# Optimization experiments

Measured on AMD Instinct MI355X. Metric: run time of the kernel, lower is better.

The kernel has to match this reference:

```python
import jax, jax.numpy as jnp
import numpy as np

EPS = 1e-5

def bn_relu(y, g, b):
    # BatchNorm1d in training mode: stats over (B, L) per channel, biased variance
    mu = jnp.mean(y, axis=(0, 2), keepdims=True)
    var = jnp.var(y, axis=(0, 2), keepdims=True)
    yn = (y - mu) * jax.lax.rsqrt(var + EPS)
    return jax.nn.relu(yn * g[None, :, None] + b[None, :, None])

def conv1x1_pad1(x, W):
    # Conv1d(k=1, padding=1, bias=False): pointwise matmul then zero-pad length by 1 each side
    y = jnp.einsum('bcl,oc->bol', x, W)
    return jnp.pad(y, ((0, 0), (0, 0), (1, 1)))

def conv1x1(x, W, b):
    return jnp.einsum('bcl,oc->bol', x, W) + b[None, :, None]

def conv3_pad1(x, W):
    # Conv1d(k=3, padding=1, bias=False); W: [O, C, 3]
    return jax.lax.conv_general_dilated(x, W, window_strides=(1,), padding=((1, 1),),
                                        dimension_numbers=('NCH', 'OIH', 'NCH'))

def pam(f, Wq, bq, Wk, bk, Wv, bv, gamma):
    q = conv1x1(f, Wq, bq)          # [B, C//8, L]
    k = conv1x1(f, Wk, bk)          # [B, C//8, L]
    v = conv1x1(f, Wv, bv)          # [B, C, L]
    energy = jnp.einsum('bql,bqm->blm', q, k)   # [B, L, L]
    attn = jax.nn.softmax(energy, axis=-1)
    out = jnp.einsum('bcm,blm->bcl', v, attn)
    return gamma * out + f

def cam(f, gamma):
    energy = jnp.einsum('bcl,bdl->bcd', f, f)    # [B, C, C]
    energy_new = jnp.max(energy, axis=-1, keepdims=True) - energy
    attn = jax.nn.softmax(energy_new, axis=-1)
    out = jnp.einsum('bcd,bdl->bcl', attn, f)
    return gamma * out + f

def setup_inputs() -> dict:
    key = jax.random.key(0)
    ks = jax.random.split(key, 24)
    B, C, L = 8, 256, 2046
    IC, OC = C // 4, 128  # inter_channels=64, out_channels
    s = 0.05
    d = {
        'x':   jax.random.normal(ks[0], (B, C, L), jnp.float32),
        'W5a': jax.random.normal(ks[1], (IC, C), jnp.float32) * s,
        'g5a': jnp.ones((IC,), jnp.float32), 'b5a': jnp.zeros((IC,), jnp.float32),
        'W5c': jax.random.normal(ks[2], (IC, C), jnp.float32) * s,
        'g5c': jnp.ones((IC,), jnp.float32), 'b5c': jnp.zeros((IC,), jnp.float32),
        'Wq':  jax.random.normal(ks[3], (IC // 8, IC), jnp.float32) * s,
        'bq':  jnp.zeros((IC // 8,), jnp.float32),
        'Wk':  jax.random.normal(ks[4], (IC // 8, IC), jnp.float32) * s,
        'bk':  jnp.zeros((IC // 8,), jnp.float32),
        'Wv':  jax.random.normal(ks[5], (IC, IC), jnp.float32) * s,
        'bv':  jnp.zeros((IC,), jnp.float32),
        'gamma_pam': jnp.full((1,), 0.1, jnp.float32),
        'gamma_cam': jnp.full((1,), 0.1, jnp.float32),
        'W51': jax.random.normal(ks[6], (IC, IC, 3), jnp.float32) * s,
        'g51': jnp.ones((IC,), jnp.float32), 'b51': jnp.zeros((IC,), jnp.float32),
        'W52': jax.random.normal(ks[7], (IC, IC, 3), jnp.float32) * s,
        'g52': jnp.ones((IC,), jnp.float32), 'b52': jnp.zeros((IC,), jnp.float32),
        'W6':  jax.random.normal(ks[8], (OC, IC), jnp.float32) * s,
        'b6':  jnp.zeros((OC,), jnp.float32),
        'W7':  jax.random.normal(ks[9], (OC, IC), jnp.float32) * s,
        'b7':  jnp.zeros((OC,), jnp.float32),
        'W8':  jax.random.normal(ks[10], (OC, IC), jnp.float32) * s,
        'b8':  jnp.zeros((OC,), jnp.float32),
    }
    return d

def reference(x, W5a, g5a, b5a, W5c, g5c, b5c, Wq, bq, Wk, bk, Wv, bv,
              gamma_pam, gamma_cam, W51, g51, b51, W52, g52, b52,
              W6, b6, W7, b7, W8, b8):
    # dropout (p=0.1) treated as identity (eval mode)
    feat1 = bn_relu(conv1x1_pad1(x, W5a), g5a, b5a)          # [B, IC, L+2]
    sa_feat = pam(feat1, Wq, bq, Wk, bk, Wv, bv, gamma_pam)
    sa_conv = bn_relu(conv3_pad1(sa_feat, W51), g51, b51)
    sa_output = conv1x1(sa_conv, W6, b6)                     # [B, OC, L+2]
    feat2 = bn_relu(conv1x1_pad1(x, W5c), g5c, b5c)
    sc_feat = cam(feat2, gamma_cam)
    sc_conv = bn_relu(conv3_pad1(sc_feat, W52), g52, b52)
    sc_output = conv1x1(sc_conv, W7, b7)
    feat_sum = sa_conv + sc_conv
    sasc = conv1x1(feat_sum, W8, b8)
    # pool == 'maxpool' selects AdaptiveAvgPool1d(1) in the original (note swap)
    sasc = jnp.mean(sasc, axis=-1)                            # [B, OC]
    return (sasc, sa_output, sc_output)
```

## Files before the change

kernel.cpp:

```cpp
#include <hip/hip_runtime.h>
#include <math.h>

#define B 8
#define C 256
#define L 2046
#define LP 2048
#define IC 64
#define OC 128
#define BN_EPS 1e-5f
#define INVN (1.f / 16384.f)

#define OFF_Y1T    0u
#define OFF_Y2C    524288u
#define OFF_SAFT   1048576u
#define OFF_SCFT   1572864u
#define OFF_Y51T   2097152u
#define OFF_Y52T   2621440u
#define OFF_VB     3145728u
#define OFF_QT     3670016u
#define OFF_KT     3735552u
#define OFF_LPART  3801088u
#define OFF_EPART  3866624u
#define OFF_ATTN   4390912u
#define OFF_PART1  4423680u
#define OFF_PART2  4489216u
#define OFF_COEF1  4554752u
#define OFF_COEF2  4555008u
#define OFF_FSUM   4555264u
#define OFF_W5BF   4555776u
#define OFF_W67    4572160u
#define OFF_WT     4580352u
#define OFF_WQKV   4592640u
#define OFF_BQKV   4595200u

typedef __attribute__((ext_vector_type(8))) short bshort8;
typedef __attribute__((ext_vector_type(4))) float f32x4;

__device__ __forceinline__ unsigned short f2bf(float f) {
    union { float f; unsigned int u; } v; v.f = f;
    unsigned int r = v.u + 0x7fffu + ((v.u >> 16) & 1u);
    return (unsigned short)(r >> 16);
}
__device__ __forceinline__ float bf2f(unsigned short u) {
    union { unsigned int i; float f; } v; v.i = ((unsigned int)u) << 16;
    return v.f;
}
__device__ __forceinline__ unsigned int pk2(float a, float b) {
    return (unsigned int)f2bf(a) | ((unsigned int)f2bf(b) << 16);
}

__global__ __launch_bounds__(256) void k_wprep(
        const float* __restrict__ W5a, const float* __restrict__ W5c,
        const float* __restrict__ W6, const float* __restrict__ W7,
        const float* __restrict__ W51, const float* __restrict__ W52,
        const float* __restrict__ Wq, const float* __restrict__ Wk,
        const float* __restrict__ Wv, const float* __restrict__ bq,
        const float* __restrict__ bk, const float* __restrict__ bv,
        unsigned short* __restrict__ W5BF, unsigned short* __restrict__ W67,
        unsigned short* __restrict__ WT, unsigned short* __restrict__ WQKV,
        float* __restrict__ BQKV, float* __restrict__ FSUM) {
    int i = blockIdx.x * 256 + threadIdx.x;
    if (i < 32768) {
        int o = i >> 8, c = i & 255;
        W5BF[i] = f2bf(o < 64 ? W5a[o * 256 + c] : W5c[(o - 64) * 256 + c]);
    } else if (i < 49152) {
        int j = i - 32768; int g = j >> 13; int r = j & 8191;
        W67[j] = f2bf(g ? W7[r] : W6[r]);
    } else if (i < 73728) {
        int j = i - 49152;
        int c = j & 63, o = (j >> 6) & 63, wt = j >> 12; int w = wt / 3, t = wt % 3;
        const float* Ws = w ? W52 : W51;
        WT[j] = f2bf(Ws[(o * 64 + c) * 3 + t]);
    } else if (i < 78848) {
        int j = i - 73728; int o = j >> 6, c = j & 63;
        float v = o < 8 ? Wq[o * 64 + c] : (o < 16 ? Wk[(o - 8) * 64 + c] : Wv[(o - 16) * 64 + c]);
        WQKV[j] = f2bf(v);
    } else if (i < 78928) {
        int o = i - 78848;
        BQKV[o] = o < 8 ? bq[o] : (o < 16 ? bk[o - 8] : bv[o - 16]);
    } else if (i < 79440) {
        FSUM[i - 78928] = 0.f;
    }
}

__global__ __launch_bounds__(256) void k_conv1(const float* __restrict__ x,
        const unsigned short* __restrict__ W5BF,
        unsigned short* __restrict__ Y1T, unsigned short* __restrict__ Y2C,
        float* __restrict__ PART1) {
    __shared__ float lds_part[4][128];
    int lt = blockIdx.x, og = blockIdx.y, b = blockIdx.z;
    int w = threadIdx.x >> 6, lane = threadIdx.x & 63;
    int n = lane & 15, quad = lane >> 4;
    int lp = lt * 64 + w * 16 + n;
    int ls = lp - 1;
    bool valid = (ls >= 0) && (ls < L);
    f32x4 acc[4];
#pragma unroll
    for (int ot = 0; ot < 4; ++ot) acc[ot] = (f32x4){0.f, 0.f, 0.f, 0.f};
    for (int ck = 0; ck < 8; ++ck) {
        int c0 = ck * 32 + quad * 8;
        bshort8 xb = {};
        if (valid) {
            const float* xs = x + ((size_t)(b * C + c0)) * L + ls;
#pragma unroll
            for (int j = 0; j < 8; ++j)
                ((unsigned short*)&xb)[j] = f2bf(xs[(size_t)j * L]);
        }
#pragma unroll
        for (int ot = 0; ot < 4; ++ot) {
            bshort8 wf = *(const bshort8*)(W5BF + (size_t)(og * 64 + ot * 16 + n) * C + ck * 32 + quad * 8);
            acc[ot] = __builtin_amdgcn_mfma_f32_16x16x32_bf16(wf, xb, acc[ot], 0, 0, 0);
        }
    }
    if (og == 0) {
#pragma unroll
        for (int ot = 0; ot < 4; ++ot) {
            uint2 pv;
            pv.x = pk2(acc[ot][0], acc[ot][1]);
            pv.y = pk2(acc[ot][2], acc[ot][3]);
            *(uint2*)(Y1T + ((size_t)(b * LP + lp)) * IC + ot * 16 + quad * 4) = pv;
        }
    } else {
#pragma unroll
        for (int ot = 0; ot < 4; ++ot)
#pragma unroll
            for (int r = 0; r < 4; ++r) {
                int o = ot * 16 + quad * 4 + r;
                Y2C[((size_t)(b * IC + o)) * LP + lp] = f2bf(acc[ot][r]);
            }
    }
#pragma unroll
    for (int ot = 0; ot < 4; ++ot)
#pragma unroll
        for (int r = 0; r < 4; ++r) {
            float s = acc[ot][r], q = s * s;
#pragma unroll
            for (int msk = 1; msk < 16; msk <<= 1) {
                s += __shfl_xor(s, msk, 64);
                q += __shfl_xor(q, msk, 64);
            }
            if (n == 0) {
                int ch = ot * 16 + quad * 4 + r;
                lds_part[w][ch * 2] = s;
                lds_part[w][ch * 2 + 1] = q;
            }
        }
    __syncthreads();
    int t = threadIdx.x;
    if (t < 128) {
        float s = lds_part[0][t] + lds_part[1][t] + lds_part[2][t] + lds_part[3][t];
        PART1[(size_t)(og * 128 + t) * 256 + (b * 32 + lt)] = s;
    }
}

__global__ __launch_bounds__(256) void k_red(const float* __restrict__ PART,
        const float* __restrict__ g0, const float* __restrict__ b0,
        const float* __restrict__ g1, const float* __restrict__ b1,
        float* __restrict__ COEF) {
    int ch = blockIdx.x;
    int t = threadIdx.x;
    float s = PART[(size_t)(ch * 2) * 256 + t];
    float q = PART[(size_t)(ch * 2 + 1) * 256 + t];
    for (int off = 32; off; off >>= 1) {
        s += __shfl_down(s, off, 64);
        q += __shfl_down(q, off, 64);
    }
    __shared__ float rs[4], rq[4];
    if ((t & 63) == 0) { rs[t >> 6] = s; rq[t >> 6] = q; }
    __syncthreads();
    if (t == 0) {
        float S = rs[0] + rs[1] + rs[2] + rs[3];
        float Q = rq[0] + rq[1] + rq[2] + rq[3];
        float mu = S * INVN;
        float var = Q * INVN - mu * mu;
        float gv = ch < 64 ? g0[ch] : g1[ch - 64];
        float bv = ch < 64 ? b0[ch] : b1[ch - 64];
        float A = gv * rsqrtf(var + BN_EPS);
        COEF[ch * 2] = A;
        COEF[ch * 2 + 1] = bv - mu * A;
    }
}

__global__ __launch_bounds__(256) void k_qkv(const unsigned short* __restrict__ Y1T,
        const float* __restrict__ COEF1,
        const unsigned short* __restrict__ WQKV, const float* __restrict__ BQKV,
        unsigned short* __restrict__ QT, unsigned short* __restrict__ KT,
        unsigned short* __restrict__ VB) {
    __shared__ float cA[64], cB[64];
    int lt = blockIdx.x, b = blockIdx.y;
    int t = threadIdx.x;
    if (t < 64) { cA[t] = COEF1[t * 2]; cB[t] = COEF1[t * 2 + 1]; }
    __syncthreads();
    int w = t >> 6, lane = t & 63, n = lane & 15, quad = lane >> 4;
    int lrow = lt * 64 + w * 16 + n;
    bshort8 fb[2];
#pragma unroll
    for (int kt = 0; kt < 2; ++kt) {
        bshort8 raw = *(const bshort8*)(Y1T + ((size_t)(b * LP + lrow)) * IC + kt * 32 + quad * 8);
        bshort8 f;
#pragma unroll
        for (int j = 0; j < 8; ++j) {
            int c = kt * 32 + quad * 8 + j;
            float v = fmaf(cA[c], bf2f((unsigned short)raw[j]), cB[c]);
            v = fmaxf(v, 0.f);
            ((unsigned short*)&f)[j] = f2bf(v);
        }
        fb[kt] = f;
    }
    f32x4 acc[5];
#pragma unroll
    for (int ot = 0; ot < 5; ++ot) {
        f32x4 a = {0.f, 0.f, 0.f, 0.f};
#pragma unroll
        for (int kt = 0; kt < 2; ++kt) {
            bshort8 wf = *(const bshort8*)(WQKV + (size_t)(ot * 16 + n) * IC + kt * 32 + quad * 8);
            a = __builtin_amdgcn_mfma_f32_16x16x32_bf16(wf, fb[kt], a, 0, 0, 0);
        }
        acc[ot] = a;
    }
#pragma unroll
    for (int ot = 0; ot < 5; ++ot)
#pragma unroll
        for (int r = 0; r < 4; ++r) {
            int o = ot * 16 + quad * 4 + r;
            unsigned short bv16 = f2bf(acc[ot][r] + BQKV[o]);
            if (ot == 0) {
                if (o < 8) QT[((size_t)(b * LP + lrow)) * 8 + o] = bv16;
                else KT[((size_t)(b * LP + lrow)) * 8 + (o - 8)] = bv16;
            } else {
                VB[((size_t)(b * IC + (o - 16))) * LP + lrow] = bv16;
            }
        }
}

__global__ __launch_bounds__(256) void k_pam(
        const unsigned short* __restrict__ qT, const unsigned short* __restrict__ kT,
        const unsigned short* __restrict__ vb,
        unsigned short* __restrict__ OPART, float* __restrict__ LPART) {
    __shared__ unsigned char smem[18432];
    unsigned short* vs = (unsigned short*)smem;
    unsigned short* ps = vs + 4608;
    float* os = (float*)smem;
    int qt = blockIdx.x, ks = blockIdx.y, b = blockIdx.z;
    int l0 = qt * 64;
    int tid = threadIdx.x;
    int wq = tid >> 6, lane = tid & 63, n = lane & 15, quad = lane >> 4;
    bshort8 qa = {};
    if (quad == 0)
        qa = *(const bshort8*)(qT + ((size_t)(b * LP + l0 + wq * 16 + n)) * 8);
    f32x4 acc[4];
#pragma unroll
    for (int s = 0; s < 4; ++s) acc[s] = (f32x4){0.f, 0.f, 0.f, 0.f};
    float li[4] = {0.f, 0.f, 0.f, 0.f};
    unsigned short* pw = ps + wq * 16 * 72;

    for (int it = 0; it < 8; ++it) {
        int m0 = ks * 512 + it * 64;
        __syncthreads();
        {
            int row = tid >> 2, chn = tid & 3;
            const unsigned short* src = vb + ((size_t)(b * IC + row)) * LP + m0 + chn * 16;
            unsigned short* dstl = vs + row * 72 + chn * 16;
            *(bshort8*)dstl = *(const bshort8*)src;
            *(bshort8*)(dstl + 8) = *(const bshort8*)(src + 8);
        }
        bshort8 kb[4];
#pragma unroll
        for (int s = 0; s < 4; ++s) kb[s] = (bshort8){};
        if (quad == 0) {
#pragma unroll
            for (int s = 0; s < 4; ++s)
                kb[s] = *(const bshort8*)(kT + ((size_t)(b * LP + m0 + s * 16 + n)) * 8);
        }
        __syncthreads();
        f32x4 sc[4];
#pragma unroll
        for (int s = 0; s < 4; ++s)
            sc[s] = __builtin_amdgcn_mfma_f32_16x16x32_bf16(qa, kb[s],
                        (f32x4){0.f, 0.f, 0.f, 0.f}, 0, 0, 0);
#pragma unroll
        for (int s = 0; s < 4; ++s)
#pragma unroll
            for (int r = 0; r < 4; ++r) {
                float p = __expf(sc[s][r]);
                li[r] += p;
                pw[(quad * 4 + r) * 72 + s * 16 + n] = f2bf(p);
            }
#pragma unroll
        for (int step = 0; step < 2; ++step) {
            bshort8 pa = *(const bshort8*)(pw + n * 72 + step * 32 + quad * 8);
#pragma unroll
            for (int s = 0; s < 4; ++s) {
                bshort8 vf = *(const bshort8*)(vs + (s * 16 + n) * 72 + step * 32 + quad * 8);
                acc[s] = __builtin_amdgcn_mfma_f32_16x16x32_bf16(pa, vf, acc[s], 0, 0, 0);
            }
        }
    }
    __syncthreads();
#pragma unroll
    for (int s = 0; s < 4; ++s)
#pragma unroll
        for (int r = 0; r < 4; ++r)
            os[(s * 16 + n) * 65 + wq * 16 + quad * 4 + r] = acc[s][r];
    size_t lbase = ((size_t)((b * 32 + qt) * 4 + ks)) * 64;
#pragma unroll
    for (int r = 0; r < 4; ++r) {
        float s_ = li[r];
#pragma unroll
        for (int msk = 1; msk < 16; msk <<= 1) s_ += __shfl_xor(s_, msk, 64);
        if (n == 0) LPART[lbase + wq * 16 + quad * 4 + r] = s_;
    }
    __syncthreads();
    size_t ob = ((size_t)((b * 32 + qt) * 4 + ks)) * 4096;
    int c = tid >> 2, qc = tid & 3;
    unsigned int* od = (unsigned int*)(OPART + ob + c * 64 + qc * 16);
#pragma unroll
    for (int i = 0; i < 8; ++i)
        od[i] = pk2(os[c * 65 + qc * 16 + 2 * i], os[c * 65 + qc * 16 + 2 * i + 1]);
}

__global__ __launch_bounds__(256) void k_pam_combine(
        const unsigned short* __restrict__ OPART, const float* __restrict__ LPART,
        const unsigned short* __restrict__ Y1T, const float* __restrict__ COEF1,
        const float* __restrict__ gamma, unsigned short* __restrict__ SAFT) {
    __shared__ float dn[64];
    __shared__ float cA[64], cB[64];
    __shared__ unsigned short tile[64 * 66];
    int qt = blockIdx.x, b = blockIdx.y;
    int l0 = qt * 64;
    int t = threadIdx.x;
    if (t < 64) {
        cA[t] = COEF1[t * 2]; cB[t] = COEF1[t * 2 + 1];
        size_t lbase = ((size_t)((b * 32 + qt) * 4)) * 64;
        dn[t] = LPART[lbase + t] + LPART[lbase + 64 + t] +
                LPART[lbase + 128 + t] + LPART[lbase + 192 + t];
    }
    __syncthreads();
    int c = t >> 2, qc = t & 3;
    float O[16];
#pragma unroll
    for (int i = 0; i < 16; ++i) O[i] = 0.f;
    size_t ob = ((size_t)((b * 32 + qt) * 4)) * 4096 + c * 64 + qc * 16;
#pragma unroll
    for (int s = 0; s < 4; ++s) {
        bshort8 p0 = *(const bshort8*)(OPART + ob + (size_t)s * 4096);
        bshort8 p1 = *(const bshort8*)(OPART + ob + (size_t)s * 4096 + 8);
#pragma unroll
        for (int i = 0; i < 8; ++i) {
            O[i]     += bf2f((unsigned short)p0[i]);
            O[8 + i] += bf2f((unsigned short)p1[i]);
        }
    }
    float gm = gamma[0];
#pragma unroll
    for (int i = 0; i < 16; ++i) {
        int q = qc * 16 + i;
        unsigned short raw = Y1T[((size_t)(b * LP + l0 + q)) * IC + c];
        float f1v = fmaxf(fmaf(cA[c], bf2f(raw), cB[c]), 0.f);
        float val = fmaf(gm, O[i] / dn[q], f1v);
        tile[q * 66 + c] = f2bf(val);
    }
    __syncthreads();
    int li = t >> 2, cc = t & 3;
    unsigned int* dst = (unsigned int*)(SAFT + ((size_t)(b * LP + l0 + li)) * IC + cc * 16);
#pragma unroll
    for (int i = 0; i < 8; ++i)
        dst[i] = *(unsigned int*)(tile + li * 66 + cc * 16 + 2 * i);
}

__global__ __launch_bounds__(256) void k_gram(const unsigned short* __restrict__ Y2C,
        const float* __restrict__ COEF1, float* __restrict__ EPART) {
    __shared__ float fs[64][132];
    __shared__ float cA[64], cB[64];
    int b = blockIdx.y;
    int l0 = blockIdx.x * 128;
    int t = threadIdx.x;
    if (t < 64) { cA[t] = COEF1[(64 + t) * 2]; cB[t] = COEF1[(64 + t) * 2 + 1]; }
    __syncthreads();
    for (int i = t; i < 64 * 64; i += 256) {
        int c = i >> 6, i2 = i & 63;
        unsigned int u = *(const unsigned int*)(Y2C + ((size_t)(b * IC + c)) * LP + l0 + i2 * 2);
        float A = cA[c], Bc = cB[c];
        fs[c][i2 * 2]     = fmaxf(fmaf(A, bf2f((unsigned short)u), Bc), 0.f);
        fs[c][i2 * 2 + 1] = fmaxf(fmaf(A, bf2f((unsigned short)(u >> 16)), Bc), 0.f);
    }
    __syncthreads();
    int c = t >> 2, dg = t & 3;
    float acc[16];
#pragma unroll
    for (int i = 0; i < 16; ++i) acc[i] = 0.f;
    for (int i4 = 0; i4 < 32; ++i4) {
        const float4 fc = *reinterpret_cast<const float4*>(&fs[c][i4 * 4]);
#pragma unroll
        for (int dd = 0; dd < 16; ++dd) {
            const float4 fd = *reinterpret_cast<const float4*>(&fs[dg * 16 + dd][i4 * 4]);
            acc[dd] += fc.x * fd.x + fc.y * fd.y + fc.z * fd.z + fc.w * fd.w;
        }
    }
    size_t base = ((size_t)(b * 16 + blockIdx.x)) * 4096 + c * 64 + dg * 16;
    for (int dd = 0; dd < 16; ++dd)
        EPART[base + dd] = acc[dd];
}

__global__ __launch_bounds__(256) void k_cam_softmax(const float* __restrict__ EPART,
        float* __restrict__ attn) {
    __shared__ float e[4096];
    int b = blockIdx.x, t = threadIdx.x;
    for (int idx = t; idx < 4096; idx += 256) {
        float s = 0.f;
        for (int ch = 0; ch < 16; ++ch) s += EPART[((size_t)(b * 16 + ch)) * 4096 + idx];
        e[idx] = s;
    }
    __syncthreads();
    if (t < 64) {
        float mn = INFINITY;
        for (int d = 0; d < 64; ++d) mn = fminf(mn, e[t * 64 + d]);
        float s = 0.f;
        float* a = attn + (size_t)b * 4096 + t * 64;
        for (int d = 0; d < 64; ++d) { float p = __expf(mn - e[t * 64 + d]); a[d] = p; s += p; }
        float inv = 1.f / s;
        for (int d = 0; d < 64; ++d) a[d] *= inv;
    }
}

__global__ __launch_bounds__(256) void k_cam_apply(const float* __restrict__ attn,
        const unsigned short* __restrict__ Y2C, const float* __restrict__ COEF1,
        const float* __restrict__ gamma, unsigned short* __restrict__ SCFT) {
    __shared__ __align__(16) float as[64 * 64];
    __shared__ float cA[64], cB[64];
    __shared__ unsigned short tile[128 * 66];
    int b = blockIdx.y;
    int l0 = blockIdx.x * 128;
    int t = threadIdx.x;
    int lq = t & 127, ch = t >> 7;
    if (t < 64) { cA[t] = COEF1[(64 + t) * 2]; cB[t] = COEF1[(64 + t) * 2 + 1]; }
    for (int i = t; i < 4096; i += 256) as[i] = attn[(size_t)b * 4096 + i];
    __syncthreads();
    float acc[32];
#pragma unroll
    for (int i = 0; i < 32; ++i) acc[i] = 0.f;
    const unsigned short* fb = Y2C + (size_t)b * IC * LP + l0 + lq;
    for (int d4 = 0; d4 < 16; ++d4) {
        float fv[4];
#pragma unroll
        for (int i = 0; i < 4; ++i) {
            int d = 4 * d4 + i;
            fv[i] = fmaxf(fmaf(cA[d], bf2f(fb[(size_t)d * LP]), cB[d]), 0.f);
        }
#pragma unroll
        for (int cc = 0; cc < 32; ++cc) {
            const float4 a4 = *reinterpret_cast<const float4*>(as + (ch * 32 + cc) * 64 + d4 * 4);
            acc[cc] += a4.x * fv[0] + a4.y * fv[1] + a4.z * fv[2] + a4.w * fv[3];
        }
    }
    float gm = gamma[0];
#pragma unroll
    for (int cc = 0; cc < 32; ++cc) {
        int c = ch * 32 + cc;
        float res = fmaxf(fmaf(cA[c], bf2f(fb[(size_t)c * LP]), cB[c]), 0.f);
        tile[lq * 66 + c] = f2bf(fmaf(gm, acc[cc], res));
    }
    __syncthreads();
    int li = t >> 1, half = t & 1;
    unsigned int* dst = (unsigned int*)(SCFT + ((size_t)(b * LP + l0 + li)) * IC + half * 32);
#pragma unroll
    for (int i = 0; i < 16; ++i)
        dst[i] = *(unsigned int*)(tile + li * 66 + half * 32 + 2 * i);
}

__global__ __launch_bounds__(256) void k_conv3(const unsigned short* __restrict__ SAFT,
        const unsigned short* __restrict__ SCFT, const unsigned short* __restrict__ WTall,
        unsigned short* __restrict__ Y51T, unsigned short* __restrict__ Y52T,
        float* __restrict__ PART2) {
    __shared__ float lds_part[4][128];
    int lt = blockIdx.x, og = blockIdx.y, b = blockIdx.z;
    const unsigned short* FTsrc = og ? SCFT : SAFT;
    const unsigned short* WT = WTall + og * 12288;
    unsigned short* dst = og ? Y52T : Y51T;
    int l0 = lt * 64;
    int w = threadIdx.x >> 6, lane = threadIdx.x & 63, n = lane & 15, quad = lane >> 4;
    int lrow = l0 + w * 16 + n;
    f32x4 acc[4];
#pragma unroll
    for (int ot = 0; ot < 4; ++ot) acc[ot] = (f32x4){0.f, 0.f, 0.f, 0.f};
#pragma unroll
    for (int t3 = 0; t3 < 3; ++t3) {
        int row = lrow + t3 - 1;
        bshort8 fb[2];
#pragma unroll
        for (int kt = 0; kt < 2; ++kt) {
            if (row >= 0 && row < LP)
                fb[kt] = *(const bshort8*)(FTsrc + ((size_t)(b * LP + row)) * IC + kt * 32 + quad * 8);
            else fb[kt] = (bshort8){};
        }
#pragma unroll
        for (int ot = 0; ot < 4; ++ot)
#pragma unroll
            for (int kt = 0; kt < 2; ++kt) {
                bshort8 wf = *(const bshort8*)(WT + ((size_t)(t3 * 64 + ot * 16 + n)) * IC + kt * 32 + quad * 8);
                acc[ot] = __builtin_amdgcn_mfma_f32_16x16x32_bf16(wf, fb[kt], acc[ot], 0, 0, 0);
            }
    }
#pragma unroll
    for (int ot = 0; ot < 4; ++ot) {
        uint2 pv;
        pv.x = pk2(acc[ot][0], acc[ot][1]);
        pv.y = pk2(acc[ot][2], acc[ot][3]);
        *(uint2*)(dst + ((size_t)(b * LP + lrow)) * IC + ot * 16 + quad * 4) = pv;
    }
#pragma unroll
    for (int ot = 0; ot < 4; ++ot)
#pragma unroll
        for (int r = 0; r < 4; ++r) {
            float s = acc[ot][r], q = s * s;
#pragma unroll
            for (int msk = 1; msk < 16; msk <<= 1) {
                s += __shfl_xor(s, msk, 64);
                q += __shfl_xor(q, msk, 64);
            }
            if (n == 0) {
                int cch = ot * 16 + quad * 4 + r;
                lds_part[w][cch * 2] = s;
                lds_part[w][cch * 2 + 1] = q;
            }
        }
    __syncthreads();
    int t = threadIdx.x;
    if (t < 128) {
        float s = lds_part[0][t] + lds_part[1][t] + lds_part[2][t] + lds_part[3][t];
        PART2[(size_t)(og * 128 + t) * 256 + (b * 32 + lt)] = s;
    }
}

__global__ __launch_bounds__(256) void k_final(const unsigned short* __restrict__ Y51T,
        const unsigned short* __restrict__ Y52T, const float* __restrict__ COEF2,
        const unsigned short* __restrict__ W67,
        const float* __restrict__ b6, const float* __restrict__ b7,
        float* __restrict__ out_sa, float* __restrict__ out_sc,
        float* __restrict__ FSUM) {
    __shared__ float cA[128], cB[128];
    __shared__ float fsw[4][64];
    int lt = blockIdx.x, og = blockIdx.y, b = blockIdx.z;
    int t = threadIdx.x;
    if (t < 128) { cA[t] = COEF2[t * 2]; cB[t] = COEF2[t * 2 + 1]; }
    __syncthreads();
    int w = t >> 6, lane = t & 63, n = lane & 15, quad = lane >> 4;
    int lrow = lt * 64 + w * 16 + n;
    float fs_lane[16];
    bshort8 ba[2], bb[2];
#pragma unroll
    for (int kt = 0; kt < 2; ++kt) {
        bshort8 ra = *(const bshort8*)(Y51T + ((size_t)(b * LP + lrow)) * IC + kt * 32 + quad * 8);
        bshort8 rb = *(const bshort8*)(Y52T + ((size_t)(b * LP + lrow)) * IC + kt * 32 + quad * 8);
        bshort8 fa, fb;
#pragma unroll
        for (int j = 0; j < 8; ++j) {
            int c = kt * 32 + quad * 8 + j;
            float v1 = fmaxf(fmaf(cA[c], bf2f((unsigned short)ra[j]), cB[c]), 0.f);
            float v2 = fmaxf(fmaf(cA[64 + c], bf2f((unsigned short)rb[j]), cB[64 + c]), 0.f);
            ((unsigned short*)&fa)[j] = f2bf(v1);
            ((unsigned short*)&fb)[j] = f2bf(v2);
            fs_lane[kt * 8 + j] = v1 + v2;
        }
        ba[kt] = fa; bb[kt] = fb;
    }
    f32x4 accA[4], accB[4];
#pragma unroll
    for (int ot = 0; ot < 4; ++ot) {
        accA[ot] = (f32x4){0.f, 0.f, 0.f, 0.f};
        accB[ot] = (f32x4){0.f, 0.f, 0.f, 0.f};
    }
#pragma unroll
    for (int ot = 0; ot < 4; ++ot)
#pragma unroll
        for (int kt = 0; kt < 2; ++kt) {
            bshort8 wa = *(const bshort8*)(W67 + (size_t)(og * 64 + ot * 16 + n) * IC + kt * 32 + quad * 8);
            bshort8 wb = *(const bshort8*)(W67 + 8192 + (size_t)(og * 64 + ot * 16 + n) * IC + kt * 32 + quad * 8);
            accA[ot] = __builtin_amdgcn_mfma_f32_16x16x32_bf16(wa, ba[kt], accA[ot], 0, 0, 0);
            accB[ot] = __builtin_amdgcn_mfma_f32_16x16x32_bf16(wb, bb[kt], accB[ot], 0, 0, 0);
        }
#pragma unroll
    for (int ot = 0; ot < 4; ++ot)
#pragma unroll
        for (int r = 0; r < 4; ++r) {
            int o = og * 64 + ot * 16 + quad * 4 + r;
            out_sa[((size_t)(b * OC + o)) * LP + lrow] = accA[ot][r] + b6[o];
            out_sc[((size_t)(b * OC + o)) * LP + lrow] = accB[ot][r] + b7[o];
        }
    if (og == 0) {
#pragma unroll
        for (int i = 0; i < 16; ++i) {
            float s = fs_lane[i];
#pragma unroll
            for (int msk = 1; msk < 16; msk <<= 1) s += __shfl_xor(s, msk, 64);
            if (n == 0) {
                int c = (i >> 3) * 32 + quad * 8 + (i & 7);
                fsw[w][c] = s;
            }
        }
        __syncthreads();
        if (t < 64)
            atomicAdd(&FSUM[b * 64 + t], fsw[0][t] + fsw[1][t] + fsw[2][t] + fsw[3][t]);
    }
}

__global__ __launch_bounds__(128) void k_sasc(const float* __restrict__ FSUM,
        const float* __restrict__ W8, const float* __restrict__ b8,
        float* __restrict__ out) {
    __shared__ float mean[64];
    int b = blockIdx.x, t = threadIdx.x;
    if (t < 64) mean[t] = FSUM[b * 64 + t] * (1.f / (float)LP);
    __syncthreads();
    float s = b8[t];
    for (int c = 0; c < 64; ++c) s = fmaf(W8[t * 64 + c], mean[c], s);
    out[b * OC + t] = s;
}

extern "C" void kernel_launch(void* const* d_in, const int* in_sizes, int n_in,
                              void* d_out, int out_size, void* d_ws, size_t ws_size,
                              hipStream_t stream) {
    (void)in_sizes; (void)n_in; (void)out_size; (void)ws_size;
    const float* x    = (const float*)d_in[0];
    const float* W5a  = (const float*)d_in[1];
    const float* g5a  = (const float*)d_in[2];
    const float* b5a  = (const float*)d_in[3];
    const float* W5c  = (const float*)d_in[4];
    const float* g5c  = (const float*)d_in[5];
    const float* b5c  = (const float*)d_in[6];
    const float* Wq   = (const float*)d_in[7];
    const float* bq   = (const float*)d_in[8];
    const float* Wk   = (const float*)d_in[9];
    const float* bk   = (const float*)d_in[10];
    const float* Wv   = (const float*)d_in[11];
    const float* bv   = (const float*)d_in[12];
    const float* gpam = (const float*)d_in[13];
    const float* gcam = (const float*)d_in[14];
    const float* W51  = (const float*)d_in[15];
    const float* g51  = (const float*)d_in[16];
    const float* b51  = (const float*)d_in[17];
    const float* W52  = (const float*)d_in[18];
    const float* g52  = (const float*)d_in[19];
    const float* b52  = (const float*)d_in[20];
    const float* W6   = (const float*)d_in[21];
    const float* b6   = (const float*)d_in[22];
    const float* W7   = (const float*)d_in[23];
    const float* b7   = (const float*)d_in[24];
    const float* W8   = (const float*)d_in[25];
    const float* b8   = (const float*)d_in[26];

    float* ws = (float*)d_ws;
    float* out = (float*)d_out;
    unsigned short* Y1T  = (unsigned short*)(ws + OFF_Y1T);
    unsigned short* Y2C  = (unsigned short*)(ws + OFF_Y2C);
    unsigned short* SAFT = (unsigned short*)(ws + OFF_SAFT);
    unsigned short* SCFT = (unsigned short*)(ws + OFF_SCFT);
    unsigned short* Y51T = (unsigned short*)(ws + OFF_Y51T);
    unsigned short* Y52T = (unsigned short*)(ws + OFF_Y52T);
    unsigned short* VB   = (unsigned short*)(ws + OFF_VB);
    unsigned short* QT   = (unsigned short*)(ws + OFF_QT);
    unsigned short* KT   = (unsigned short*)(ws + OFF_KT);
    float* LPART  = ws + OFF_LPART;
    float* EPART  = ws + OFF_EPART;
    float* ATTN   = ws + OFF_ATTN;
    float* PART1  = ws + OFF_PART1;
    float* PART2  = ws + OFF_PART2;
    float* COEF1  = ws + OFF_COEF1;
    float* COEF2  = ws + OFF_COEF2;
    float* FSUM   = ws + OFF_FSUM;
    unsigned short* W5BF = (unsigned short*)(ws + OFF_W5BF);
    unsigned short* W67  = (unsigned short*)(ws + OFF_W67);
    unsigned short* WT   = (unsigned short*)(ws + OFF_WT);
    unsigned short* WQKV = (unsigned short*)(ws + OFF_WQKV);
    float* BQKV = ws + OFF_BQKV;

    float* out_sa = out + B * OC;
    float* out_sc = out + B * OC + (size_t)B * OC * LP;
    unsigned short* OPART = (unsigned short*)out_sa;

    k_wprep<<<311, 256, 0, stream>>>(W5a, W5c, W6, W7, W51, W52, Wq, Wk, Wv,
                                     bq, bk, bv, W5BF, W67, WT, WQKV, BQKV, FSUM);
    k_conv1<<<dim3(32, 2, B), 256, 0, stream>>>(x, W5BF, Y1T, Y2C, PART1);
    k_red<<<128, 256, 0, stream>>>(PART1, g5a, b5a, g5c, b5c, COEF1);
    k_qkv<<<dim3(32, B), 256, 0, stream>>>(Y1T, COEF1, WQKV, BQKV, QT, KT, VB);
    k_pam<<<dim3(32, 4, B), 256, 0, stream>>>(QT, KT, VB, OPART, LPART);
    k_pam_combine<<<dim3(32, B), 256, 0, stream>>>(OPART, LPART, Y1T, COEF1, gpam, SAFT);
    k_gram<<<dim3(16, B), 256, 0, stream>>>(Y2C, COEF1, EPART);
    k_cam_softmax<<<B, 256, 0, stream>>>(EPART, ATTN);
    k_cam_apply<<<dim3(16, B), 256, 0, stream>>>(ATTN, Y2C, COEF1, gcam, SCFT);
    k_conv3<<<dim3(32, 2, B), 256, 0, stream>>>(SAFT, SCFT, WT, Y51T, Y52T, PART2);
    k_red<<<128, 256, 0, stream>>>(PART2, g51, b51, g52, b52, COEF2);
    k_final<<<dim3(32, 2, B), 256, 0, stream>>>(Y51T, Y52T, COEF2, W67, b6, b7,
                                                out_sa, out_sc, FSUM);
    k_sasc<<<B, 128, 0, stream>>>(FSUM, W8, b8, out);
}
```

Baseline: 243.4 us.

## Fuse independent PAM/CAM stages into shared launches and drop reduction kernels

Replaces the per-tile BN partial buffers and the two k_red kernels with atomic accumulation of channel sums, with each consumer computing the BN coefficients itself. Independent PAM and CAM work (qkv+gram, pam+cam_softmax, pam_combine+cam_apply) now runs as role-dispatched blocks inside single launches using dynamic shared memory. The gram step is rewritten to use bf16 MFMA instead of fp32 FMA, and the final sasc mean is folded into k_final via atomics. Together these cut the launch count from 13 to 7 and let independent branches fill the GPU concurrently. In exchange, float atomics make the sums order-nondeterministic and the bf16 gram adds rounding error.

Result: faster. 233.5 us (-4.1%).

```diff
diff --git a/kernel.cpp b/kernel.cpp
--- a/kernel.cpp
+++ b/kernel.cpp
@@ -22,16 +22,13 @@
 #define OFF_LPART  3801088u
 #define OFF_EPART  3866624u
 #define OFF_ATTN   4390912u
-#define OFF_PART1  4423680u
-#define OFF_PART2  4489216u
-#define OFF_COEF1  4554752u
-#define OFF_COEF2  4555008u
-#define OFF_FSUM   4555264u
-#define OFF_W5BF   4555776u
-#define OFF_W67    4572160u
-#define OFF_WT     4580352u
-#define OFF_WQKV   4592640u
-#define OFF_BQKV   4595200u
+#define OFF_STATS1 4423680u
+#define OFF_STATS2 4423936u
+#define OFF_W5BF   4424192u
+#define OFF_W67    4440576u
+#define OFF_WT     4448768u
+#define OFF_WQKV   4461056u
+#define OFF_BQKV   4463616u
 
 typedef __attribute__((ext_vector_type(8))) short bshort8;
 typedef __attribute__((ext_vector_type(4))) float f32x4;
@@ -47,6 +44,20 @@
 }
 __device__ __forceinline__ unsigned int pk2(float a, float b) {
     return (unsigned int)f2bf(a) | ((unsigned int)f2bf(b) << 16);
+}
+
+__device__ __forceinline__ void load_coef(const float* __restrict__ STATS,
+        const float* __restrict__ g, const float* __restrict__ beta,
+        int base, int cnt, float* cA, float* cB) {
+    int t = threadIdx.x;
+    if (t < cnt) {
+        float s = STATS[(base + t) * 2], q = STATS[(base + t) * 2 + 1];
+        float mu = s * INVN;
+        float var = q * INVN - mu * mu;
+        float A = g[t] * rsqrtf(var + BN_EPS);
+        cA[t] = A;
+        cB[t] = beta[t] - mu * A;
+    }
 }
 
 __global__ __launch_bounds__(256) void k_wprep(
@@ -56,9 +67,11 @@
         const float* __restrict__ Wq, const float* __restrict__ Wk,
         const float* __restrict__ Wv, const float* __restrict__ bq,
         const float* __restrict__ bk, const float* __restrict__ bv,
+        const float* __restrict__ b8,
         unsigned short* __restrict__ W5BF, unsigned short* __restrict__ W67,
         unsigned short* __restrict__ WT, unsigned short* __restrict__ WQKV,
-        float* __restrict__ BQKV, float* __restrict__ FSUM) {
+        float* __restrict__ BQKV, float* __restrict__ STATS1,
+        float* __restrict__ STATS2, float* __restrict__ out_sasc) {
     int i = blockIdx.x * 256 + threadIdx.x;
     if (i < 32768) {
         int o = i >> 8, c = i & 255;
@@ -76,17 +89,21 @@
         float v = o < 8 ? Wq[o * 64 + c] : (o < 16 ? Wk[(o - 8) * 64 + c] : Wv[(o - 16) * 64 + c]);
         WQKV[j] = f2bf(v);
     } else if (i < 78928) {
-        int o = i - 78848;
+        int o = i - 73728 - 5120;
         BQKV[o] = o < 8 ? bq[o] : (o < 16 ? bk[o - 8] : bv[o - 16]);
     } else if (i < 79440) {
-        FSUM[i - 78928] = 0.f;
+        int j = i - 78928;
+        if (j < 256) STATS1[j] = 0.f; else STATS2[j - 256] = 0.f;
+    } else if (i < 80464) {
+        int j = i - 79440;
+        out_sasc[j] = b8[j & 127];
     }
 }
 
 __global__ __launch_bounds__(256) void k_conv1(const float* __restrict__ x,
         const unsigned short* __restrict__ W5BF,
         unsigned short* __restrict__ Y1T, unsigned short* __restrict__ Y2C,
-        float* __restrict__ PART1) {
+        float* __restrict__ STATS1) {
     __shared__ float lds_part[4][128];
     int lt = blockIdx.x, og = blockIdx.y, b = blockIdx.z;
     int w = threadIdx.x >> 6, lane = threadIdx.x & 63;
@@ -149,48 +166,21 @@
     int t = threadIdx.x;
     if (t < 128) {
         float s = lds_part[0][t] + lds_part[1][t] + lds_part[2][t] + lds_part[3][t];
-        PART1[(size_t)(og * 128 + t) * 256 + (b * 32 + lt)] = s;
-    }
-}
-
-__global__ __launch_bounds__(256) void k_red(const float* __restrict__ PART,
-        const float* __restrict__ g0, const float* __restrict__ b0,
-        const float* __restrict__ g1, const float* __restrict__ b1,
-        float* __restrict__ COEF) {
-    int ch = blockIdx.x;
-    int t = threadIdx.x;
-    float s = PART[(size_t)(ch * 2) * 256 + t];
-    float q = PART[(size_t)(ch * 2 + 1) * 256 + t];
-    for (int off = 32; off; off >>= 1) {
-        s += __shfl_down(s, off, 64);
-        q += __shfl_down(q, off, 64);
-    }
-    __shared__ float rs[4], rq[4];
-    if ((t & 63) == 0) { rs[t >> 6] = s; rq[t >> 6] = q; }
-    __syncthreads();
-    if (t == 0) {
-        float S = rs[0] + rs[1] + rs[2] + rs[3];
-        float Q = rq[0] + rq[1] + rq[2] + rq[3];
-        float mu = S * INVN;
-        float var = Q * INVN - mu * mu;
-        float gv = ch < 64 ? g0[ch] : g1[ch - 64];
-        float bv = ch < 64 ? b0[ch] : b1[ch - 64];
-        float A = gv * rsqrtf(var + BN_EPS);
-        COEF[ch * 2] = A;
-        COEF[ch * 2 + 1] = bv - mu * A;
-    }
-}
-
-__global__ __launch_bounds__(256) void k_qkv(const unsigned short* __restrict__ Y1T,
-        const float* __restrict__ COEF1,
+        atomicAdd(&STATS1[og * 128 + t], s);
+    }
+}
+
+__device__ void role_qkv(char* dynsm, int lt, int b,
+        const unsigned short* __restrict__ Y1T, const float* __restrict__ STATS1,
+        const float* __restrict__ g5a, const float* __restrict__ b5a,
         const unsigned short* __restrict__ WQKV, const float* __restrict__ BQKV,
         unsigned short* __restrict__ QT, unsigned short* __restrict__ KT,
         unsigned short* __restrict__ VB) {
-    __shared__ float cA[64], cB[64];
-    int lt = blockIdx.x, b = blockIdx.y;
-    int t = threadIdx.x;
-    if (t < 64) { cA[t] = COEF1[t * 2]; cB[t] = COEF1[t * 2 + 1]; }
-    __syncthreads();
+    float* cA = (float*)dynsm;
+    float* cB = cA + 64;
+    load_coef(STATS1, g5a, b5a, 0, 64, cA, cB);
+    __syncthreads();
+    int t = threadIdx.x;
     int w = t >> 6, lane = t & 63, n = lane & 15, quad = lane >> 4;
     int lrow = lt * 64 + w * 16 + n;
     bshort8 fb[2];
@@ -201,8 +191,7 @@
 #pragma unroll
         for (int j = 0; j < 8; ++j) {
             int c = kt * 32 + quad * 8 + j;
-            float v = fmaf(cA[c], bf2f((unsigned short)raw[j]), cB[c]);
-            v = fmaxf(v, 0.f);
+            float v = fmaxf(fmaf(cA[c], bf2f((unsigned short)raw[j]), cB[c]), 0.f);
             ((unsigned short*)&f)[j] = f2bf(v);
         }
         fb[kt] = f;
@@ -233,15 +222,73 @@
         }
 }
 
-__global__ __launch_bounds__(256) void k_pam(
+__device__ void role_gram(char* dynsm, int blk, int b,
+        const unsigned short* __restrict__ Y2C, const float* __restrict__ STATS1,
+        const float* __restrict__ g5c, const float* __restrict__ b5c,
+        float* __restrict__ EPART) {
+    float* cA = (float*)dynsm;
+    float* cB = cA + 64;
+    load_coef(STATS1, g5c, b5c, 64, 64, cA, cB);
+    __syncthreads();
+    int t = threadIdx.x;
+    int w = t >> 6, lane = t & 63, n = lane & 15, quad = lane >> 4;
+    f32x4 acc[4][4];
+#pragma unroll
+    for (int ti = 0; ti < 4; ++ti)
+#pragma unroll
+        for (int tj = 0; tj < 4; ++tj) acc[ti][tj] = (f32x4){0.f, 0.f, 0.f, 0.f};
+    for (int chunk = 0; chunk < 4; ++chunk) {
+        int lb = (blk * 4 + w) * 128 + chunk * 32 + quad * 8;
+        bshort8 frag[4];
+#pragma unroll
+        for (int g = 0; g < 4; ++g) {
+            int c = g * 16 + n;
+            bshort8 raw = *(const bshort8*)(Y2C + ((size_t)(b * IC + c)) * LP + lb);
+            bshort8 f;
+            float A = cA[c], Bc = cB[c];
+#pragma unroll
+            for (int j = 0; j < 8; ++j)
+                ((unsigned short*)&f)[j] = f2bf(fmaxf(fmaf(A, bf2f((unsigned short)raw[j]), Bc), 0.f));
+            frag[g] = f;
+        }
+#pragma unroll
+        for (int ti = 0; ti < 4; ++ti)
+#pragma unroll
+            for (int tj = 0; tj < 4; ++tj)
+                acc[ti][tj] = __builtin_amdgcn_mfma_f32_16x16x32_bf16(frag[ti], frag[tj], acc[ti][tj], 0, 0, 0);
+    }
+    float* ep = EPART + ((size_t)(b * 16 + blk * 4 + w)) * 4096;
+#pragma unroll
+    for (int ti = 0; ti < 4; ++ti)
+#pragma unroll
+        for (int tj = 0; tj < 4; ++tj)
+#pragma unroll
+            for (int r = 0; r < 4; ++r)
+                ep[(ti * 16 + quad * 4 + r) * 64 + tj * 16 + n] = acc[ti][tj][r];
+}
+
+__global__ __launch_bounds__(256) void k_fuse1(
+        const unsigned short* __restrict__ Y1T, const unsigned short* __restrict__ Y2C,
+        const float* __restrict__ STATS1,
+        const float* __restrict__ g5a, const float* __restrict__ b5a,
+        const float* __restrict__ g5c, const float* __restrict__ b5c,
+        const unsigned short* __restrict__ WQKV, const float* __restrict__ BQKV,
+        unsigned short* __restrict__ QT, unsigned short* __restrict__ KT,
+        unsigned short* __restrict__ VB, float* __restrict__ EPART) {
+    extern __shared__ char dynsm[];
+    int idx = blockIdx.x;
+    if (idx < 256) role_qkv(dynsm, idx & 31, idx >> 5, Y1T, STATS1, g5a, b5a,
+                            WQKV, BQKV, QT, KT, VB);
+    else { int g = idx - 256; role_gram(dynsm, g & 3, g >> 2, Y2C, STATS1, g5c, b5c, EPART); }
+}
+
+__device__ void role_pam(char* dynsm, int qt, int ks, int b,
         const unsigned short* __restrict__ qT, const unsigned short* __restrict__ kT,
         const unsigned short* __restrict__ vb,
         unsigned short* __restrict__ OPART, float* __restrict__ LPART) {
-    __shared__ unsigned char smem[18432];
-    unsigned short* vs = (unsigned short*)smem;
+    unsigned short* vs = (unsigned short*)dynsm;
     unsigned short* ps = vs + 4608;
-    float* os = (float*)smem;
-    int qt = blockIdx.x, ks = blockIdx.y, b = blockIdx.z;
+    float* os = (float*)dynsm;
     int l0 = qt * 64;
     int tid = threadIdx.x;
     int wq = tid >> 6, lane = tid & 63, n = lane & 15, quad = lane >> 4;
@@ -319,93 +366,10 @@
         od[i] = pk2(os[c * 65 + qc * 16 + 2 * i], os[c * 65 + qc * 16 + 2 * i + 1]);
 }
 
-__global__ __launch_bounds__(256) void k_pam_combine(
-        const unsigned short* __restrict__ OPART, const float* __restrict__ LPART,
-        const unsigned short* __restrict__ Y1T, const float* __restrict__ COEF1,
-        const float* __restrict__ gamma, unsigned short* __restrict__ SAFT) {
-    __shared__ float dn[64];
-    __shared__ float cA[64], cB[64];
-    __shared__ unsigned short tile[64 * 66];
-    int qt = blockIdx.x, b = blockIdx.y;
-    int l0 = qt * 64;
-    int t = threadIdx.x;
-    if (t < 64) {
-        cA[t] = COEF1[t * 2]; cB[t] = COEF1[t * 2 + 1];
-        size_t lbase = ((size_t)((b * 32 + qt) * 4)) * 64;
-        dn[t] = LPART[lbase + t] + LPART[lbase + 64 + t] +
-                LPART[lbase + 128 + t] + LPART[lbase + 192 + t];
-    }
-    __syncthreads();
-    int c = t >> 2, qc = t & 3;
-    float O[16];
-#pragma unroll
-    for (int i = 0; i < 16; ++i) O[i] = 0.f;
-    size_t ob = ((size_t)((b * 32 + qt) * 4)) * 4096 + c * 64 + qc * 16;
-#pragma unroll
-    for (int s = 0; s < 4; ++s) {
-        bshort8 p0 = *(const bshort8*)(OPART + ob + (size_t)s * 4096);
-        bshort8 p1 = *(const bshort8*)(OPART + ob + (size_t)s * 4096 + 8);
-#pragma unroll
-        for (int i = 0; i < 8; ++i) {
-            O[i]     += bf2f((unsigned short)p0[i]);
-            O[8 + i] += bf2f((unsigned short)p1[i]);
-        }
-    }
-    float gm = gamma[0];
-#pragma unroll
-    for (int i = 0; i < 16; ++i) {
-        int q = qc * 16 + i;
-        unsigned short raw = Y1T[((size_t)(b * LP + l0 + q)) * IC + c];
-        float f1v = fmaxf(fmaf(cA[c], bf2f(raw), cB[c]), 0.f);
-        float val = fmaf(gm, O[i] / dn[q], f1v);
-        tile[q * 66 + c] = f2bf(val);
-    }
-    __syncthreads();
-    int li = t >> 2, cc = t & 3;
-    unsigned int* dst = (unsigned int*)(SAFT + ((size_t)(b * LP + l0 + li)) * IC + cc * 16);
-#pragma unroll
-    for (int i = 0; i < 8; ++i)
-        dst[i] = *(unsigned int*)(tile + li * 66 + cc * 16 + 2 * i);
-}
-
-__global__ __launch_bounds__(256) void k_gram(const unsigned short* __restrict__ Y2C,
-        const float* __restrict__ COEF1, float* __restrict__ EPART) {
-    __shared__ float fs[64][132];
-    __shared__ float cA[64], cB[64];
-    int b = blockIdx.y;
-    int l0 = blockIdx.x * 128;
-    int t = threadIdx.x;
-    if (t < 64) { cA[t] = COEF1[(64 + t) * 2]; cB[t] = COEF1[(64 + t) * 2 + 1]; }
-    __syncthreads();
-    for (int i = t; i < 64 * 64; i += 256) {
-        int c = i >> 6, i2 = i & 63;
-        unsigned int u = *(const unsigned int*)(Y2C + ((size_t)(b * IC + c)) * LP + l0 + i2 * 2);
-        float A = cA[c], Bc = cB[c];
-        fs[c][i2 * 2]     = fmaxf(fmaf(A, bf2f((unsigned short)u), Bc), 0.f);
-        fs[c][i2 * 2 + 1] = fmaxf(fmaf(A, bf2f((unsigned short)(u >> 16)), Bc), 0.f);
-    }
-    __syncthreads();
-    int c = t >> 2, dg = t & 3;
-    float acc[16];
-#pragma unroll
-    for (int i = 0; i < 16; ++i) acc[i] = 0.f;
-    for (int i4 = 0; i4 < 32; ++i4) {
-        const float4 fc = *reinterpret_cast<const float4*>(&fs[c][i4 * 4]);
-#pragma unroll
-        for (int dd = 0; dd < 16; ++dd) {
-            const float4 fd = *reinterpret_cast<const float4*>(&fs[dg * 16 + dd][i4 * 4]);
-            acc[dd] += fc.x * fd.x + fc.y * fd.y + fc.z * fd.z + fc.w * fd.w;
-        }
-    }
-    size_t base = ((size_t)(b * 16 + blockIdx.x)) * 4096 + c * 64 + dg * 16;
-    for (int dd = 0; dd < 16; ++dd)
-        EPART[base + dd] = acc[dd];
-}
-
-__global__ __launch_bounds__(256) void k_cam_softmax(const float* __restrict__ EPART,
-        float* __restrict__ attn) {
-    __shared__ float e[4096];
-    int b = blockIdx.x, t = threadIdx.x;
+__device__ void role_cam_softmax(char* dynsm, int b,
+        const float* __restrict__ EPART, float* __restrict__ attn) {
+    float* e = (float*)dynsm;
+    int t = threadIdx.x;
     for (int idx = t; idx < 4096; idx += 256) {
         float s = 0.f;
         for (int ch = 0; ch < 16; ++ch) s += EPART[((size_t)(b * 16 + ch)) * 4096 + idx];
@@ -423,17 +387,80 @@
     }
 }
 
-__global__ __launch_bounds__(256) void k_cam_apply(const float* __restrict__ attn,
-        const unsigned short* __restrict__ Y2C, const float* __restrict__ COEF1,
+__global__ __launch_bounds__(256) void k_fuse2(
+        const unsigned short* __restrict__ QT, const unsigned short* __restrict__ KT,
+        const unsigned short* __restrict__ VB,
+        unsigned short* __restrict__ OPART, float* __restrict__ LPART,
+        const float* __restrict__ EPART, float* __restrict__ ATTN) {
+    extern __shared__ char dynsm[];
+    int idx = blockIdx.x;
+    if (idx < 1024) role_pam(dynsm, idx & 31, (idx >> 5) & 3, idx >> 7, QT, KT, VB, OPART, LPART);
+    else role_cam_softmax(dynsm, idx - 1024, EPART, ATTN);
+}
+
+__device__ void role_pam_combine(char* dynsm, int qt, int b,
+        const unsigned short* __restrict__ OPART, const float* __restrict__ LPART,
+        const unsigned short* __restrict__ Y1T, const float* __restrict__ STATS1,
+        const float* __restrict__ g5a, const float* __restrict__ b5a,
+        const float* __restrict__ gamma, unsigned short* __restrict__ SAFT) {
+    float* dn = (float*)dynsm;
+    float* cA = dn + 64;
+    float* cB = cA + 64;
+    unsigned short* tile = (unsigned short*)(cB + 64);
+    int l0 = qt * 64;
+    int t = threadIdx.x;
+    load_coef(STATS1, g5a, b5a, 0, 64, cA, cB);
+    if (t < 64) {
+        size_t lbase = ((size_t)((b * 32 + qt) * 4)) * 64;
+        dn[t] = LPART[lbase + t] + LPART[lbase + 64 + t] +
+                LPART[lbase + 128 + t] + LPART[lbase + 192 + t];
+    }
+    __syncthreads();
+    int c = t >> 2, qc = t & 3;
+    float O[16];
+#pragma unroll
+    for (int i = 0; i < 16; ++i) O[i] = 0.f;
+    size_t ob = ((size_t)((b * 32 + qt) * 4)) * 4096 + c * 64 + qc * 16;
+#pragma unroll
+    for (int s = 0; s < 4; ++s) {
+        bshort8 p0 = *(const bshort8*)(OPART + ob + (size_t)s * 4096);
+        bshort8 p1 = *(const bshort8*)(OPART + ob + (size_t)s * 4096 + 8);
+#pragma unroll
+        for (int i = 0; i < 8; ++i) {
+            O[i]     += bf2f((unsigned short)p0[i]);
+            O[8 + i] += bf2f((unsigned short)p1[i]);
+        }
+    }
+    float gm = gamma[0];
+#pragma unroll
+    for (int i = 0; i < 16; ++i) {
+        int q = qc * 16 + i;
+        unsigned short raw = Y1T[((size_t)(b * LP + l0 + q)) * IC + c];
+        float f1v = fmaxf(fmaf(cA[c], bf2f(raw), cB[c]), 0.f);
+        float val = fmaf(gm, O[i] / dn[q], f1v);
+        tile[q * 66 + c] = f2bf(val);
+    }
+    __syncthreads();
+    int li = t >> 2, cc = t & 3;
+    unsigned int* dst = (unsigned int*)(SAFT + ((size_t)(b * LP + l0 + li)) * IC + cc * 16);
+#pragma unroll
+    for (int i = 0; i < 8; ++i)
+        dst[i] = *(unsigned int*)(tile + li * 66 + cc * 16 + 2 * i);
+}
+
+__device__ void role_cam_apply(char* dynsm, int blkx, int b,
+        const float* __restrict__ attn, const unsigned short* __restrict__ Y2C,
+        const float* __restrict__ STATS1,
+        const float* __restrict__ g5c, const float* __restrict__ b5c,
         const float* __restrict__ gamma, unsigned short* __restrict__ SCFT) {
-    __shared__ __align__(16) float as[64 * 64];
-    __shared__ float cA[64], cB[64];
-    __shared__ unsigned short tile[128 * 66];
-    int b = blockIdx.y;
-    int l0 = blockIdx.x * 128;
+    float* as = (float*)dynsm;
+    float* cA = as + 4096;
+    float* cB = cA + 64;
+    unsigned short* tile = (unsigned short*)(cB + 64);
+    int l0 = blkx * 128;
     int t = threadIdx.x;
     int lq = t & 127, ch = t >> 7;
-    if (t < 64) { cA[t] = COEF1[(64 + t) * 2]; cB[t] = COEF1[(64 + t) * 2 + 1]; }
+    load_coef(STATS1, g5c, b5c, 64, 64, cA, cB);
     for (int i = t; i < 4096; i += 256) as[i] = attn[(size_t)b * 4096 + i];
     __syncthreads();
     float acc[32];
@@ -468,10 +495,27 @@
         dst[i] = *(unsigned int*)(tile + li * 66 + half * 32 + 2 * i);
 }
 
+__global__ __launch_bounds__(256) void k_fuse3(
+        const unsigned short* __restrict__ OPART, const float* __restrict__ LPART,
+        const unsigned short* __restrict__ Y1T, const unsigned short* __restrict__ Y2C,
+        const float* __restrict__ STATS1,
+        const float* __restrict__ g5a, const float* __restrict__ b5a,
+        const float* __restrict__ g5c, const float* __restrict__ b5c,
+        const float* __restrict__ gpam, const float* __restrict__ gcam,
+        const float* __restrict__ ATTN,
+        unsigned short* __restrict__ SAFT, unsigned short* __restrict__ SCFT) {
+    extern __shared__ char dynsm[];
+    int idx = blockIdx.x;
+    if (idx < 256) role_pam_combine(dynsm, idx & 31, idx >> 5, OPART, LPART, Y1T,
+                                    STATS1, g5a, b5a, gpam, SAFT);
+    else { int g = idx - 256; role_cam_apply(dynsm, g & 15, g >> 4, ATTN, Y2C,
+                                             STATS1, g5c, b5c, gcam, SCFT); }
+}
+
 __global__ __launch_bounds__(256) void k_conv3(const unsigned short* __restrict__ SAFT,
         const unsigned short* __restrict__ SCFT, const unsigned short* __restrict__ WTall,
         unsigned short* __restrict__ Y51T, unsigned short* __restrict__ Y52T,
-        float* __restrict__ PART2) {
+        float* __restrict__ STATS2) {
     __shared__ float lds_part[4][128];
     int lt = blockIdx.x, og = blockIdx.y, b = blockIdx.z;
     const unsigned short* FTsrc = og ? SCFT : SAFT;
@@ -528,21 +572,38 @@
     int t = threadIdx.x;
     if (t < 128) {
         float s = lds_part[0][t] + lds_part[1][t] + lds_part[2][t] + lds_part[3][t];
-        PART2[(size_t)(og * 128 + t) * 256 + (b * 32 + lt)] = s;
+        atomicAdd(&STATS2[og * 128 + t], s);
     }
 }
 
 __global__ __launch_bounds__(256) void k_final(const unsigned short* __restrict__ Y51T,
-        const unsigned short* __restrict__ Y52T, const float* __restrict__ COEF2,
+        const unsigned short* __restrict__ Y52T, const float* __restrict__ STATS2,
+        const float* __restrict__ g51, const float* __restrict__ b51,
+        const float* __restrict__ g52, const float* __restrict__ b52,
         const unsigned short* __restrict__ W67,
         const float* __restrict__ b6, const float* __restrict__ b7,
+        const float* __restrict__ W8,
         float* __restrict__ out_sa, float* __restrict__ out_sc,
-        float* __restrict__ FSUM) {
+        float* __restrict__ out_sasc) {
     __shared__ float cA[128], cB[128];
     __shared__ float fsw[4][64];
+    __shared__ float chsum[64];
     int lt = blockIdx.x, og = blockIdx.y, b = blockIdx.z;
     int t = threadIdx.x;
-    if (t < 128) { cA[t] = COEF2[t * 2]; cB[t] = COEF2[t * 2 + 1]; }
+    {
+        if (t < 64) {
+            float s = STATS2[t * 2], q = STATS2[t * 2 + 1];
+            float mu = s * INVN, var = q * INVN - mu * mu;
+            float A = g51[t] * rsqrtf(var + BN_EPS);
+            cA[t] = A; cB[t] = b51[t] - mu * A;
+        } else if (t < 128) {
+            int c = t - 64;
+            float s = STATS2[t * 2], q = STATS2[t * 2 + 1];
+            float mu = s * INVN, var = q * INVN - mu * mu;
+            float A = g52[c] * rsqrtf(var + BN_EPS);
+            cA[t] = A; cB[t] = b52[c] - mu * A;
+        }
+    }
     __syncthreads();
     int w = t >> 6, lane = t & 63, n = lane & 15, quad = lane >> 4;
     int lrow = lt * 64 + w * 16 + n;
@@ -599,21 +660,14 @@
             }
         }
         __syncthreads();
-        if (t < 64)
-            atomicAdd(&FSUM[b * 64 + t], fsw[0][t] + fsw[1][t] + fsw[2][t] + fsw[3][t]);
-    }
-}
-
-__global__ __launch_bounds__(128) void k_sasc(const float* __restrict__ FSUM,
-        const float* __restrict__ W8, const float* __restrict__ b8,
-        float* __restrict__ out) {
-    __shared__ float mean[64];
-    int b = blockIdx.x, t = threadIdx.x;
-    if (t < 64) mean[t] = FSUM[b * 64 + t] * (1.f / (float)LP);
-    __syncthreads();
-    float s = b8[t];
-    for (int c = 0; c < 64; ++c) s = fmaf(W8[t * 64 + c], mean[c], s);
-    out[b * OC + t] = s;
+        if (t < 64) chsum[t] = fsw[0][t] + fsw[1][t] + fsw[2][t] + fsw[3][t];
+        __syncthreads();
+        if (t < 128) {
+            float s = 0.f;
+            for (int c = 0; c < 64; ++c) s = fmaf(W8[t * 64 + c], chsum[c], s);
+            atomicAdd(&out_sasc[b * OC + t], s * (1.f / (float)LP));
+        }
+    }
 }
 
 extern "C" void kernel_launch(void* const* d_in, const int* in_sizes, int n_in,
@@ -662,11 +716,8 @@
     float* LPART  = ws + OFF_LPART;
     float* EPART  = ws + OFF_EPART;
     float* ATTN   = ws + OFF_ATTN;
-    float* PART1  = ws + OFF_PART1;
-    float* PART2  = ws + OFF_PART2;
-    float* COEF1  = ws + OFF_COEF1;
-    float* COEF2  = ws + OFF_COEF2;
-    float* FSUM   = ws + OFF_FSUM;
+    float* STATS1 = ws + OFF_STATS1;
+    float* STATS2 = ws + OFF_STATS2;
     unsigned short* W5BF = (unsigned short*)(ws + OFF_W5BF);
     unsigned short* W67  = (unsigned short*)(ws + OFF_W67);
     unsigned short* WT   = (unsigned short*)(ws + OFF_WT);
@@ -677,19 +728,17 @@
     float* out_sc = out + B * OC + (size_t)B * OC * LP;
     unsigned short* OPART = (unsigned short*)out_sa;
 
-    k_wprep<<<311, 256, 0, stream>>>(W5a, W5c, W6, W7, W51, W52, Wq, Wk, Wv,
-                                     bq, bk, bv, W5BF, W67, WT, WQKV, BQKV, FSUM);
-    k_conv1<<<dim3(32, 2, B), 256, 0, stream>>>(x, W5BF, Y1T, Y2C, PART1);
-    k_red<<<128, 256, 0, stream>>>(PART1, g5a, b5a, g5c, b5c, COEF1);
-    k_qkv<<<dim3(32, B), 256, 0, stream>>>(Y1T, COEF1, WQKV, BQKV, QT, KT, VB);
-    k_pam<<<dim3(32, 4, B), 256, 0, stream>>>(QT, KT, VB, OPART, LPART);
-    k_pam_combine<<<dim3(32, B), 256, 0, stream>>>(OPART, LPART, Y1T, COEF1, gpam, SAFT);
-    k_gram<<<dim3(16, B), 256, 0, stream>>>(Y2C, COEF1, EPART);
-    k_cam_softmax<<<B, 256, 0, stream>>>(EPART, ATTN);
-    k_cam_apply<<<dim3(16, B), 256, 0, stream>>>(ATTN, Y2C, COEF1, gcam, SCFT);
-    k_conv3<<<dim3(32, 2, B), 256, 0, stream>>>(SAFT, SCFT, WT, Y51T, Y52T, PART2);
-    k_red<<<128, 256, 0, stream>>>(PART2, g51, b51, g52, b52, COEF2);
-    k_final<<<dim3(32, 2, B), 256, 0, stream>>>(Y51T, Y52T, COEF2, W67, b6, b7,
-                                                out_sa, out_sc, FSUM);
-    k_sasc<<<B, 128, 0, stream>>>(FSUM, W8, b8, out);
-}
+    k_wprep<<<315, 256, 0, stream>>>(W5a, W5c, W6, W7, W51, W52, Wq, Wk, Wv,
+                                     bq, bk, bv, b8, W5BF, W67, WT, WQKV, BQKV,
+                                     STATS1, STATS2, out);
+    k_conv1<<<dim3(32, 2, B), 256, 0, stream>>>(x, W5BF, Y1T, Y2C, STATS1);
+    k_fuse1<<<288, 256, 512, stream>>>(Y1T, Y2C, STATS1, g5a, b5a, g5c, b5c,
+                                       WQKV, BQKV, QT, KT, VB, EPART);
+    k_fuse2<<<1032, 256, 18432, stream>>>(QT, KT, VB, OPART, LPART, EPART, ATTN);
+    k_fuse3<<<384, 256, 33792, stream>>>(OPART, LPART, Y1T, Y2C, STATS1,
+                                         g5a, b5a, g5c, b5c, gpam, gcam, ATTN,
+                                         SAFT, SCFT);
+    k_conv3<<<dim3(32, 2, B), 256, 0, stream>>>(SAFT, SCFT, WT, Y51T, Y52T, STATS2);
+    k_final<<<dim3(32, 2, B), 256, 0, stream>>>(Y51T, Y52T, STATS2, g51, b51, g52, b52,
+                                                W67, b6, b7, W8, out_sa, out_sc, out);
+}
```
